# Kernel tuning notes

Measured on AMD Instinct MI355X. Metric: run time of the kernel, lower is better.

The kernel has to match this reference:

```python
import jax, jax.numpy as jnp
import numpy as np

B, T, D, HD = 8, 2048, 768, 64

def setup_inputs() -> dict:
    key = jax.random.key(0)
    k1, k2, k3, k4 = jax.random.split(key, 4)
    scale = 1.0 / np.sqrt(D)
    return {
        "x": jax.random.normal(k1, (B, T, D), dtype=jnp.float32),
        "Wq": jax.random.normal(k2, (D, HD), dtype=jnp.float32) * scale,
        "Wk": jax.random.normal(k3, (D, HD), dtype=jnp.float32) * scale,
        "Wv": jax.random.normal(k4, (D, HD), dtype=jnp.float32) * scale,
    }

def reference(x, Wq, Wk, Wv):
    # q,k,v: [B,T,HD]
    q = jnp.einsum('btd,dh->bth', x, Wq)
    k = jnp.einsum('btd,dh->bth', x, Wk)
    v = jnp.einsum('btd,dh->bth', x, Wv)
    dk = q.shape[-1]
    # scores: [B,T,T], scaled then causally masked with -inf
    scores = jnp.einsum('bqh,bkh->bqk', q, k) / jnp.sqrt(jnp.float32(dk))
    Tq = scores.shape[-1]
    causal = jnp.tril(jnp.ones((Tq, Tq), dtype=bool))
    scores = jnp.where(causal, scores, -jnp.inf)
    attn = jax.nn.softmax(scores, axis=-1)  # dropout rate 0 (eval mode)
    return jnp.einsum('bqk,bkh->bqh', attn, v)
```

## Files before the change

kernel.cpp:

```cpp
#include <hip/hip_runtime.h>
#include <hip/hip_bf16.h>
#include <stdint.h>

#define B_  8
#define T_  2048
#define D_  768
#define HD_ 64
#define M_  (B_ * T_)

typedef short s16x8 __attribute__((ext_vector_type(8)));
typedef float f32x4 __attribute__((ext_vector_type(4)));
typedef float f32x16 __attribute__((ext_vector_type(16)));
typedef unsigned int u32;

union Frag { uint4 u; s16x8 h; };

__device__ __forceinline__ unsigned short f2bf(float f) {
    unsigned u = __builtin_bit_cast(unsigned, f);
    u += 0x7FFFu + ((u >> 16) & 1u);
    return (unsigned short)(u >> 16);
}
__device__ __forceinline__ unsigned pack_bf16x2(float lo, float hi) {
    return (unsigned)f2bf(lo) | ((unsigned)f2bf(hi) << 16);
}
__device__ __forceinline__ unsigned cvt_pk(float lo, float hi) {
    unsigned r;
    asm("v_cvt_pk_bf16_f32 %0, %1, %2" : "=v"(r) : "v"(lo), "v"(hi));
    return r;
}

__device__ __forceinline__ void gl_lds16(const void* g, void* l) {
    __builtin_amdgcn_global_load_lds(
        (const __attribute__((address_space(1))) u32*)g,
        (__attribute__((address_space(3))) u32*)l, 16, 0, 0);
}

__global__ __launch_bounds__(64) void prep_pk(const float* __restrict__ Wq,
                                              const float* __restrict__ Wk,
                                              const float* __restrict__ Wv,
                                              unsigned short* __restrict__ pk) {
    int nb = blockIdx.x / 24, kk = blockIdx.x % 24;
    int lane = threadIdx.x, g = lane >> 4, t = lane & 15;
    int mat = nb >> 2, col = (nb & 3) * 16 + t;
    const float* W = (mat == 0) ? Wq : (mat == 1) ? Wk : Wv;
    float s = (mat == 0) ? 0.18033688011112042f : 1.0f;
    float v[8];
#pragma unroll
    for (int e = 0; e < 8; e++)
        v[e] = W[(size_t)(kk * 32 + g * 8 + e) * HD_ + col] * s;
    uint4 u;
    u.x = pack_bf16x2(v[0], v[1]);
    u.y = pack_bf16x2(v[2], v[3]);
    u.z = pack_bf16x2(v[4], v[5]);
    u.w = pack_bf16x2(v[6], v[7]);
    *(uint4*)(pk + ((size_t)blockIdx.x * 64 + lane) * 8) = u;
}

__global__ __launch_bounds__(256, 2) void qkv_proj(const float* __restrict__ x,
                                                   const unsigned short* __restrict__ pk,
                                                   unsigned short* __restrict__ qo,
                                                   unsigned short* __restrict__ ko,
                                                   unsigned short* __restrict__ vt) {
    __shared__ char xs[4][8192];

    int tid = threadIdx.x, w = tid >> 6, lane = tid & 63;
    int g = lane >> 4, t = lane & 15;
    int m0 = blockIdx.x * 32;

    auto STAGE = [&](int jb) {
        int buf = jb & 3;
#pragma unroll
        for (int h = 0; h < 2; h++) {
            int s = tid + h * 256;
            int row = s >> 4;
            int a = (s & 15) ^ (row & 15);
            gl_lds16(x + (size_t)(m0 + row) * D_ + jb * 64 + a * 4,
                     &xs[buf][(w * 64 + h * 256) * 16]);
        }
    };

    const unsigned short* wp = pk + (size_t)w * 36864;
    auto LOADB = [&](Frag (&bb)[6], int jb) {
#pragma unroll
        for (int j = 0; j < 3; j++)
#pragma unroll
            for (int c = 0; c < 2; c++)
                bb[j * 2 + c].u = *(const uint4*)(wp + ((size_t)(j * 24 + jb * 2 + c) * 64 + lane) * 8);
    };

    f32x4 acc[3][2];
#pragma unroll
    for (int j = 0; j < 3; j++)
#pragma unroll
        for (int mf = 0; mf < 2; mf++) acc[j][mf] = (f32x4){0.f, 0.f, 0.f, 0.f};

    Frag bfr[3][6];
    LOADB(bfr[0], 0);
    LOADB(bfr[1], 1);
    STAGE(0); STAGE(1); STAGE(2);

#pragma unroll
    for (int jb = 0; jb < 12; jb++) {
        if (jb + 2 < 12) LOADB(bfr[(jb + 2) % 3], jb + 2);
        if (jb == 0)       asm volatile("s_waitcnt vmcnt(10)" ::: "memory");
        else if (jb == 10) asm volatile("s_waitcnt vmcnt(8)"  ::: "memory");
        else if (jb == 11) asm volatile("s_waitcnt vmcnt(0)"  ::: "memory");
        else               asm volatile("s_waitcnt vmcnt(16)" ::: "memory");
        __builtin_amdgcn_s_barrier();
        int buf = jb & 3;

        Frag af[2][2];
#pragma unroll
        for (int mf = 0; mf < 2; mf++) {
            int r32 = mf * 16 + t;
#pragma unroll
            for (int c = 0; c < 2; c++) {
                float4 f0 = *(const float4*)(&xs[buf][r32 * 256 + (((c * 8 + g * 2 + 0) ^ t) * 16)]);
                float4 f1 = *(const float4*)(&xs[buf][r32 * 256 + (((c * 8 + g * 2 + 1) ^ t) * 16)]);
                af[mf][c].u.x = cvt_pk(f0.x, f0.y);
                af[mf][c].u.y = cvt_pk(f0.z, f0.w);
                af[mf][c].u.z = cvt_pk(f1.x, f1.y);
                af[mf][c].u.w = cvt_pk(f1.z, f1.w);
            }
        }
        __builtin_amdgcn_s_setprio(1);
#pragma unroll
        for (int j = 0; j < 3; j++)
#pragma unroll
            for (int c = 0; c < 2; c++) {
                acc[j][0] = __builtin_amdgcn_mfma_f32_16x16x32_bf16(af[0][c].h, bfr[jb % 3][j * 2 + c].h, acc[j][0], 0, 0, 0);
                acc[j][1] = __builtin_amdgcn_mfma_f32_16x16x32_bf16(af[1][c].h, bfr[jb % 3][j * 2 + c].h, acc[j][1], 0, 0, 0);
            }
        __builtin_amdgcn_s_setprio(0);
        __builtin_amdgcn_s_barrier();
        if (jb + 3 < 12) STAGE(jb + 3);
    }

#pragma unroll
    for (int j = 0; j < 3; j++) {
        int nb = w * 3 + j;
        int col = (nb & 3) * 16 + t;
#pragma unroll
        for (int mf = 0; mf < 2; mf++) {
            int row0 = m0 + mf * 16;
            if (nb < 8) {
                unsigned short* dst = (nb < 4) ? qo : ko;
#pragma unroll
                for (int r = 0; r < 4; r++)
                    dst[(size_t)(row0 + g * 4 + r) * HD_ + col] = f2bf(acc[j][mf][r]);
            } else {
                int bb = m0 >> 11;
                int trow = (row0 & 2047) + g * 4;
                uint2 pkk;
                pkk.x = cvt_pk(acc[j][mf][0], acc[j][mf][1]);
                pkk.y = cvt_pk(acc[j][mf][2], acc[j][mf][3]);
                *(uint2*)(vt + (((size_t)(bb * HD_ + col)) << 11) + trow) = pkk;
            }
        }
    }
}

__global__ __launch_bounds__(256) void attn(const unsigned short* __restrict__ qw,
                                            const unsigned short* __restrict__ kw,
                                            const unsigned short* __restrict__ vt,
                                            float* __restrict__ out) {
    __shared__ char smem[65536];

    int tid = threadIdx.x, wv = tid >> 6, lane = tid & 63;
    int hi = lane >> 5, l31 = lane & 31;
    int blk = blockIdx.x;
    int b = blk & 7, idx = blk >> 3;
    int qblk = (idx < 32) ? (63 - idx) : (idx - 32);
    int q0 = qblk * 32;
    int qg = q0 + l31;
    size_t bbase = (size_t)b * T_;
    int nt = qblk + 1;
    int ks = wv;
    int mt = (nt > ks) ? ((nt - ks + 3) >> 2) : 0;

    const unsigned short* kp = kw + bbase * HD_;
    const unsigned short* vp = vt + ((size_t)(b * HD_) << 11);
    char* KV = smem + wv * 16384;

    Frag qf[4];
#pragma unroll
    for (int c = 0; c < 4; c++)
        qf[c].u = *(const uint4*)(qw + (bbase + qg) * HD_ + c * 16 + hi * 8);

    auto STAGE = [&](int j, int buf) {
        int kv0 = j * 32;
#pragma unroll
        for (int q = 0; q < 4; q++) {
            int kr = q * 8 + (lane >> 3);
            int ka = (lane & 7) ^ (kr & 7);
            gl_lds16(kp + (size_t)(kv0 + kr) * HD_ + ka * 8, KV + buf * 4096 + q * 1024);
        }
#pragma unroll
        for (int q = 0; q < 4; q++) {
            int vd = q * 16 + (lane >> 2);
            int va = (lane & 3) ^ (vd & 3) ^ ((vd >> 2) & 3);
            gl_lds16(vp + ((size_t)vd << 11) + kv0 + va * 8, KV + 8192 + buf * 4096 + q * 1024);
        }
    };

    f32x16 o0, o1;
#pragma unroll
    for (int r = 0; r < 16; r++) { o0[r] = 0.f; o1[r] = 0.f; }
    float lacc = 0.f;

    auto QK = [&](const char* KB, f32x16& st) {
#pragma unroll
        for (int r = 0; r < 16; r++) st[r] = 0.f;
        __builtin_amdgcn_s_setprio(1);
#pragma unroll
        for (int c = 0; c < 4; c++) {
            Frag ka;
            ka.u = *(const uint4*)(KB + l31 * 128 + (((c * 2 + hi) ^ (l31 & 7)) * 16));
            st = __builtin_amdgcn_mfma_f32_32x32x16_bf16(ka.h, qf[c].h, st, 0, 0, 0);
        }
        __builtin_amdgcn_s_setprio(0);
    };

    auto SMPV = [&](f32x16& st, int j, const char* VB) {
        int kv0 = j * 32;
        if (j == qblk) {
#pragma unroll
            for (int r = 0; r < 16; r++) {
                int key = kv0 + (r & 3) + 8 * (r >> 2) + 4 * hi;
                if (key > qg) st[r] = -1e30f;
            }
        }
        float p[16], ss = 0.f;
#pragma unroll
        for (int r = 0; r < 16; r++) { p[r] = exp2f(st[r]); ss += p[r]; }
        lacc += ss;

        u32 A0 = cvt_pk(p[0], p[1]),   A1 = cvt_pk(p[2], p[3]);
        u32 B0 = cvt_pk(p[4], p[5]),   B1 = cvt_pk(p[6], p[7]);
        u32 C0 = cvt_pk(p[8], p[9]),   C1 = cvt_pk(p[10], p[11]);
        u32 D0 = cvt_pk(p[12], p[13]), D1 = cvt_pk(p[14], p[15]);
        u32 A0x = (u32)__shfl_xor((int)A0, 32);
        u32 A1x = (u32)__shfl_xor((int)A1, 32);
        u32 B0x = (u32)__shfl_xor((int)B0, 32);
        u32 B1x = (u32)__shfl_xor((int)B1, 32);
        u32 C0x = (u32)__shfl_xor((int)C0, 32);
        u32 C1x = (u32)__shfl_xor((int)C1, 32);
        u32 D0x = (u32)__shfl_xor((int)D0, 32);
        u32 D1x = (u32)__shfl_xor((int)D1, 32);
        Frag pf0, pf1;
        pf0.u.x = hi ? B0x : A0;
        pf0.u.y = hi ? B1x : A1;
        pf0.u.z = hi ? B0  : A0x;
        pf0.u.w = hi ? B1  : A1x;
        pf1.u.x = hi ? D0x : C0;
        pf1.u.y = hi ? D1x : C1;
        pf1.u.z = hi ? D0  : C0x;
        pf1.u.w = hi ? D1  : C1x;

        __builtin_amdgcn_s_setprio(1);
        {
            int sw0 = (l31 & 3) ^ ((l31 >> 2) & 3);
            Frag va;
            va.u = *(const uint4*)(VB + l31 * 64 + (((hi) ^ sw0) * 16));
            o0 = __builtin_amdgcn_mfma_f32_32x32x16_bf16(va.h, pf0.h, o0, 0, 0, 0);
            va.u = *(const uint4*)(VB + l31 * 64 + (((2 + hi) ^ sw0) * 16));
            o0 = __builtin_amdgcn_mfma_f32_32x32x16_bf16(va.h, pf1.h, o0, 0, 0, 0);
            int d1 = 32 + l31;
            int sw1 = (d1 & 3) ^ ((d1 >> 2) & 3);
            va.u = *(const uint4*)(VB + d1 * 64 + (((hi) ^ sw1) * 16));
            o1 = __builtin_amdgcn_mfma_f32_32x32x16_bf16(va.h, pf0.h, o1, 0, 0, 0);
            va.u = *(const uint4*)(VB + d1 * 64 + (((2 + hi) ^ sw1) * 16));
            o1 = __builtin_amdgcn_mfma_f32_32x32x16_bf16(va.h, pf1.h, o1, 0, 0, 0);
        }
        __builtin_amdgcn_s_setprio(0);
    };

    if (mt > 0) STAGE(ks, 0);
    if (mt > 1) STAGE(ks + 4, 1);

    int i = 0;
#pragma unroll 1
    for (; i + 2 <= mt; i += 2) {
        int ja = ks + 4 * i, jb2 = ja + 4;
        const char* KA = KV + (i & 1) * 4096;
        const char* VA = KV + 8192 + (i & 1) * 4096;
        const char* KB2 = KV + ((i + 1) & 1) * 4096;
        const char* VB2 = KV + 8192 + ((i + 1) & 1) * 4096;

        asm volatile("s_waitcnt vmcnt(12)" ::: "memory");
        f32x16 sa;
        QK(KA, sa);
        asm volatile("s_waitcnt vmcnt(4)" ::: "memory");
        f32x16 sb;
        QK(KB2, sb);
        SMPV(sa, ja, VA);
        asm volatile("s_waitcnt vmcnt(0)" ::: "memory");
        if (i + 2 < mt) STAGE(ks + 4 * (i + 2), i & 1);
        SMPV(sb, jb2, VB2);
        if (i + 3 < mt) STAGE(ks + 4 * (i + 3), (i + 1) & 1);
    }
    if (i < mt) {
        int ja = ks + 4 * i;
        const char* KA = KV + (i & 1) * 4096;
        const char* VA = KV + 8192 + (i & 1) * 4096;
        asm volatile("s_waitcnt vmcnt(4)" ::: "memory");
        f32x16 sa;
        QK(KA, sa);
        asm volatile("s_waitcnt vmcnt(0)" ::: "memory");
        SMPV(sa, ja, VA);
    }

    asm volatile("s_waitcnt vmcnt(0)" ::: "memory");
    __syncthreads();

    lacc += __shfl_xor(lacc, 32);
    float* MO = (float*)smem;
    if (wv) {
        int base = ((wv - 1) * 64 + lane) * 33;
#pragma unroll
        for (int r = 0; r < 16; r++) { MO[base + r] = o0[r]; MO[base + 16 + r] = o1[r]; }
        MO[base + 32] = lacc;
    }
    __syncthreads();
    if (wv == 0) {
        float ls = lacc;
#pragma unroll
        for (int k = 0; k < 3; k++) ls += MO[(k * 64 + lane) * 33 + 32];
        float inv = 1.0f / ls;
        float* op = out + (bbase + qg) * HD_;
#pragma unroll
        for (int r = 0; r < 16; r++) {
            float s0 = o0[r], s1 = o1[r];
#pragma unroll
            for (int k = 0; k < 3; k++) {
                s0 += MO[(k * 64 + lane) * 33 + r];
                s1 += MO[(k * 64 + lane) * 33 + 16 + r];
            }
            int dr = (r & 3) + 8 * (r >> 2) + 4 * hi;
            op[dr] = s0 * inv;
            op[32 + dr] = s1 * inv;
        }
    }
}

extern "C" void kernel_launch(void* const* d_in, const int* in_sizes, int n_in,
                              void* d_out, int out_size, void* d_ws, size_t ws_size,
                              hipStream_t stream) {
    const float* x  = (const float*)d_in[0];
    const float* Wq = (const float*)d_in[1];
    const float* Wk = (const float*)d_in[2];
    const float* Wv = (const float*)d_in[3];
    char* ws = (char*)d_ws;
    unsigned short* pkw = (unsigned short*)ws;
    unsigned short* qw = (unsigned short*)(ws + 294912);
    unsigned short* kw = (unsigned short*)(ws + 294912 + 2097152);
    unsigned short* vt = (unsigned short*)(ws + 294912 + 4194304);
    float* out = (float*)d_out;

    hipLaunchKernelGGL(prep_pk, dim3(288), dim3(64), 0, stream, Wq, Wk, Wv, pkw);
    hipLaunchKernelGGL(qkv_proj, dim3(M_ / 32), dim3(256), 0, stream, x, pkw, qw, kw, vt);
    hipLaunchKernelGGL(attn, dim3(512), dim3(256), 0, stream, qw, kw, vt, out);
}
```

Before: 42.34 us.

## Drop projection loop barrier, clamp KV staging index, parallelize attention epilogue reduction

In the QKV projection GEMM, the next tile is now staged right after the first barrier and the second per-iteration barrier is removed, so staging overlaps the MFMA work. This assumes a four-deep LDS ring stays race-free with lookahead three. The attention kernel clamps the KV tile index during staging so prefetches past the causal limit stay in bounds. The final cross-wave reduction now spreads across all waves with vectorized float4 LDS writes and coalesced float4 global stores, replacing the serial reduction in wave 0.

```diff
diff --git a/kernel.cpp b/kernel.cpp
--- a/kernel.cpp
+++ b/kernel.cpp
@@ -107,6 +107,7 @@
         else if (jb == 11) asm volatile("s_waitcnt vmcnt(0)"  ::: "memory");
         else               asm volatile("s_waitcnt vmcnt(16)" ::: "memory");
         __builtin_amdgcn_s_barrier();
+        if (jb + 3 < 12) STAGE(jb + 3);
         int buf = jb & 3;
 
         Frag af[2][2];
@@ -132,8 +133,6 @@
                 acc[j][1] = __builtin_amdgcn_mfma_f32_16x16x32_bf16(af[1][c].h, bfr[jb % 3][j * 2 + c].h, acc[j][1], 0, 0, 0);
             }
         __builtin_amdgcn_s_setprio(0);
-        __builtin_amdgcn_s_barrier();
-        if (jb + 3 < 12) STAGE(jb + 3);
     }
 
 #pragma unroll
@@ -188,7 +187,8 @@
         qf[c].u = *(const uint4*)(qw + (bbase + qg) * HD_ + c * 16 + hi * 8);
 
     auto STAGE = [&](int j, int buf) {
-        int kv0 = j * 32;
+        int jj = (j < nt) ? j : (nt - 1);
+        int kv0 = jj * 32;
 #pragma unroll
         for (int q = 0; q < 4; q++) {
             int kr = q * 8 + (lane >> 3);
@@ -311,35 +311,48 @@
     }
 
     asm volatile("s_waitcnt vmcnt(0)" ::: "memory");
+    lacc += __shfl_xor(lacc, 32);
     __syncthreads();
 
-    lacc += __shfl_xor(lacc, 32);
     float* MO = (float*)smem;
-    if (wv) {
-        int base = ((wv - 1) * 64 + lane) * 33;
-#pragma unroll
-        for (int r = 0; r < 16; r++) { MO[base + r] = o0[r]; MO[base + 16 + r] = o1[r]; }
+    {
+        int base = (wv * 64 + lane) * 36;
+#pragma unroll
+        for (int qd = 0; qd < 4; qd++) {
+            float4 w4;
+            w4.x = o0[qd * 4 + 0]; w4.y = o0[qd * 4 + 1];
+            w4.z = o0[qd * 4 + 2]; w4.w = o0[qd * 4 + 3];
+            *(float4*)&MO[base + qd * 4] = w4;
+            float4 v4;
+            v4.x = o1[qd * 4 + 0]; v4.y = o1[qd * 4 + 1];
+            v4.z = o1[qd * 4 + 2]; v4.w = o1[qd * 4 + 3];
+            *(float4*)&MO[base + 16 + qd * 4] = v4;
+        }
         MO[base + 32] = lacc;
     }
     __syncthreads();
-    if (wv == 0) {
-        float ls = lacc;
-#pragma unroll
-        for (int k = 0; k < 3; k++) ls += MO[(k * 64 + lane) * 33 + 32];
-        float inv = 1.0f / ls;
-        float* op = out + (bbase + qg) * HD_;
-#pragma unroll
-        for (int r = 0; r < 16; r++) {
-            float s0 = o0[r], s1 = o1[r];
-#pragma unroll
-            for (int k = 0; k < 3; k++) {
-                s0 += MO[(k * 64 + lane) * 33 + r];
-                s1 += MO[(k * 64 + lane) * 33 + 16 + r];
-            }
-            int dr = (r & 3) + 8 * (r >> 2) + 4 * hi;
-            op[dr] = s0 * inv;
-            op[32 + dr] = s1 * inv;
-        }
+    {
+        int row = tid >> 3;
+        int c0 = (tid & 7) * 8;
+        int j0 = 4 * ((c0 & 31) >> 3) + ((c0 >> 5) << 4);
+        float lsum = 0.f;
+#pragma unroll
+        for (int k = 0; k < 4; k++) lsum += MO[(k * 64 + row) * 36 + 32];
+        float inv = 1.0f / lsum;
+        float4 aq = {0.f, 0.f, 0.f, 0.f};
+        float4 bq = {0.f, 0.f, 0.f, 0.f};
+#pragma unroll
+        for (int k = 0; k < 4; k++) {
+            float4 v0 = *(const float4*)&MO[(k * 64 + row) * 36 + j0];
+            float4 v1 = *(const float4*)&MO[(k * 64 + row + 32) * 36 + j0];
+            aq.x += v0.x; aq.y += v0.y; aq.z += v0.z; aq.w += v0.w;
+            bq.x += v1.x; bq.y += v1.y; bq.z += v1.z; bq.w += v1.w;
+        }
+        aq.x *= inv; aq.y *= inv; aq.z *= inv; aq.w *= inv;
+        bq.x *= inv; bq.y *= inv; bq.z *= inv; bq.w *= inv;
+        float* op = out + (bbase + q0 + row) * HD_ + c0;
+        *(float4*)&op[0] = aq;
+        *(float4*)&op[4] = bq;
     }
 }
 
```

Result: no change. 41.99 us (median of 3 runs) (-0.8%).
